# Performance work log

Measured on AMD Instinct MI355X. Metric: run time of the kernel, lower is better.

Reference implementation:

```python
import jax, jax.numpy as jnp
import numpy as np


def _quantize(mat):
    # per-row (last-dim) symmetric int8 quantization; scale stored in fp16 like torch
    max_val = (jnp.max(jnp.abs(mat), axis=-1) / 127.0).astype(jnp.float16)
    # torch's .to(int8) truncates toward zero; jnp astype does the same for in-range values
    q = (mat / max_val[..., None].astype(mat.dtype)).astype(jnp.int8)
    return q, max_val


def setup_inputs() -> dict:
    key = jax.random.key(0)
    k1, k2, k3, k4 = jax.random.split(key, 4)
    B, S, D_IN, D_OUT = 4, 2048, 4096, 4096
    x = jax.random.normal(k1, (B, S, D_IN), dtype=jnp.float32)
    origin_weight = jax.random.normal(k2, (D_OUT, D_IN), dtype=jnp.float32) * 0.02
    bias = jax.random.normal(k3, (D_OUT,), dtype=jnp.float32) * 0.01
    act_max = jax.random.normal(k4, (D_IN,), dtype=jnp.float32)
    return {"x": x, "origin_weight": origin_weight, "bias": bias,
            "act_max": act_max, "alpha": 32}


def reference(x, origin_weight, bias, act_max, alpha):
    d_in = act_max.shape[-1]
    # get_unq_idx_topk: top-alpha outlier channels by |act_max|
    _, idx = jax.lax.top_k(jnp.abs(act_max), alpha)          # [alpha]
    t = jnp.ones((d_in,), dtype=origin_weight.dtype).at[idx].set(0)

    # weight decomposition + quantization (done in __init__ in torch)
    weight_q, w_max = _quantize(origin_weight * t)           # [out,in] int8, [out] fp16
    weight_unq = origin_weight[:, idx].T                      # [alpha, out]

    # activation decomposition + per-token quantization
    x_unq = x[..., idx]                                       # [B,S,alpha]
    x_q, x_max = _quantize(x * t.astype(x.dtype))             # [B,S,in] int8, [B,S] fp16

    # simulated MatMulInteger: int8 values multiplied in fp32
    res_q = jnp.matmul(x_q.astype(jnp.float32), weight_q.T.astype(jnp.float32))  # [B,S,out]
    mx = (x_max[..., None] * w_max[None, :]).astype(jnp.float32)                  # [B,S,out]
    res_q = (res_q * mx).astype(x.dtype)

    # fp outlier path
    res_unq = jnp.matmul(x_unq, weight_unq) + bias
    return res_q + res_unq
```

## Files before the change

### kernel.cpp

```cpp
#include <hip/hip_runtime.h>
#include <hip/hip_fp16.h>

typedef __attribute__((ext_vector_type(4)))  int   i32x4;
typedef __attribute__((ext_vector_type(16))) int   i32x16;

#define ALPHA 32
#define BM 256
#define BN 128
#define BK 128


__global__ __launch_bounds__(256) void topk_kernel(const float* __restrict__ act_max,
                                                   int* __restrict__ idx_out,
                                                   unsigned* __restrict__ tbits,
                                                   int K) {
  __shared__ float v[4096];
  __shared__ float rv[4];
  __shared__ int   ri[4];
  __shared__ unsigned bits[128];
  const int t = threadIdx.x;
  for (int i = t; i < K; i += 256) v[i] = fabsf(act_max[i]);
  for (int i = t; i < K / 32; i += 256) bits[i] = 0xFFFFFFFFu;
  __syncthreads();
  for (int sel = 0; sel < ALPHA; ++sel) {
    float bv = -1.f; int bi = 0;
    for (int i = t; i < K; i += 256) {
      float x = v[i];
      if (x > bv) { bv = x; bi = i; }
    }
    for (int m = 1; m < 64; m <<= 1) {
      float ov = __shfl_xor(bv, m);
      int   oi = __shfl_xor(bi, m);
      if (ov > bv || (ov == bv && oi < bi)) { bv = ov; bi = oi; }
    }
    if ((t & 63) == 0) { rv[t >> 6] = bv; ri[t >> 6] = bi; }
    __syncthreads();
    if (t == 0) {
      for (int u = 1; u < 4; ++u)
        if (rv[u] > bv || (rv[u] == bv && ri[u] < bi)) { bv = rv[u]; bi = ri[u]; }
      idx_out[sel] = bi;
      v[bi] = -2.f;
      bits[bi >> 5] &= ~(1u << (bi & 31));
    }
    __syncthreads();
  }
  for (int i = t; i < K / 32; i += 256) tbits[i] = bits[i];
}

__global__ __launch_bounds__(256) void quant_rows_kernel(
    const float* __restrict__ src, const unsigned* __restrict__ tbits,
    const int* __restrict__ idx, signed char* __restrict__ q,
    _Float16* __restrict__ smax, float* __restrict__ unq, int K, int R) {
  __shared__ unsigned bits[128];
  __shared__ float red[4];
  const int t = threadIdx.x;
  const int r = blockIdx.x;
  for (int i = t; i < K / 32; i += 256) bits[i] = tbits[i];
  __syncthreads();
  const float4* srow = (const float4*)(src + (size_t)r * K);
  float4 vals[4];
  float am = 0.f;
#pragma unroll
  for (int j = 0; j < 4; ++j) {
    int p = 4 * t + j;
    float4 v = srow[p];
    int k0 = p << 2;
    unsigned b = bits[k0 >> 5] >> (k0 & 31);
    if (!(b & 1u)) v.x = 0.f;
    if (!(b & 2u)) v.y = 0.f;
    if (!(b & 4u)) v.z = 0.f;
    if (!(b & 8u)) v.w = 0.f;
    vals[j] = v;
    am = fmaxf(am, fmaxf(fmaxf(fabsf(v.x), fabsf(v.y)), fmaxf(fabsf(v.z), fabsf(v.w))));
  }
#pragma unroll
  for (int m = 1; m < 64; m <<= 1) am = fmaxf(am, __shfl_xor(am, m));
  if ((t & 63) == 0) red[t >> 6] = am;
  __syncthreads();
  am = fmaxf(fmaxf(red[0], red[1]), fmaxf(red[2], red[3]));
  const _Float16 sh = (_Float16)(am / 127.0f);
  const float s = (float)sh;
  if (t == 0) smax[r] = sh;
  union { signed char c[16]; int4 v; } o;
#pragma unroll
  for (int j = 0; j < 4; ++j) {
    float4 v = vals[j];
    o.c[4 * j + 0] = (signed char)(v.x / s);
    o.c[4 * j + 1] = (signed char)(v.y / s);
    o.c[4 * j + 2] = (signed char)(v.z / s);
    o.c[4 * j + 3] = (signed char)(v.w / s);
  }
  *(int4*)(q + (size_t)(r >> 5) * 32 * K + (size_t)t * 512 + (r & 31) * 16) = o.v;
  if (t < ALPHA) unq[(size_t)t * R + r] = src[(size_t)r * K + idx[t]];
}

__device__ __forceinline__ void gld_lds16(const signed char* g, signed char* l) {
  __builtin_amdgcn_global_load_lds(
      (const __attribute__((address_space(1))) void*)g,
      (__attribute__((address_space(3))) void*)l, 16, 0, 0);
}

__global__ __launch_bounds__(256, 2) void gemm_kernel(
    const signed char* __restrict__ xq, const signed char* __restrict__ wq,
    const _Float16* __restrict__ xmax, const _Float16* __restrict__ wmax,
    const float* __restrict__ xuf,
    const float* __restrict__ wuf,
    const float* __restrict__ bias,
    float* __restrict__ out, int M, int N, int K) {
  __shared__ union {
    struct { signed char A[BM * BK]; signed char B[BN * BK]; } g;
    struct { float xu[ALPHA * BM]; float wu[ALPHA * BN]; } e;
  } sm;
  __shared__ _Float16 xmh[BM];
  __shared__ _Float16 wmh[BN];
  __shared__ float    bl[BN];

  const int t = threadIdx.x;
  const int bid = blockIdx.y * gridDim.x + blockIdx.x;
  const int xcd = bid & 7, loc = bid >> 3;
  const int bxi = xcd * 4 + (loc & 3);
  const int byi = loc >> 2;
  const int bm0 = byi * BM;
  const int bn0 = bxi * BN;
  const int lane = t & 63, w = t >> 6;
  const int wm = w >> 1, wn = w & 1;
  const int hi = lane >> 5, l31 = lane & 31;

  i32x16 acc[4][2] = {};

  const signed char* aSrc = xq + (size_t)bm0 * K + 16 * t;
  const signed char* bSrc = wq + (size_t)bn0 * K + 16 * t;
  signed char* aDst = sm.g.A + t * 16;
  signed char* bDst = sm.g.B + t * 16;

  for (int k0 = 0; k0 < K; k0 += BK) {
    __syncthreads();
    const size_t koff = (size_t)k0 * 32;
#pragma unroll
    for (int i = 0; i < 8; ++i) gld_lds16(aSrc + (size_t)i * 32 * K + koff, aDst + i * 4096);
#pragma unroll
    for (int i = 0; i < 4; ++i) gld_lds16(bSrc + (size_t)i * 32 * K + koff, bDst + i * 4096);
    __syncthreads();
    const signed char* aRd = sm.g.A + 16 * lane + 4096 * (wm * 4);
    const signed char* bRd = sm.g.B + 16 * lane + 4096 * (wn * 2);
#pragma unroll
    for (int ks = 0; ks < 4; ++ks) {
      i32x4 af[4], bf[2];
#pragma unroll
      for (int mi = 0; mi < 4; ++mi)
        af[mi] = *(const i32x4*)(aRd + mi * 4096 + ks * 1024);
#pragma unroll
      for (int ni = 0; ni < 2; ++ni)
        bf[ni] = *(const i32x4*)(bRd + ni * 4096 + ks * 1024);
#pragma unroll
      for (int mi = 0; mi < 4; ++mi)
#pragma unroll
        for (int ni = 0; ni < 2; ++ni)
          acc[mi][ni] = __builtin_amdgcn_mfma_i32_32x32x32_i8(af[mi], bf[ni], acc[mi][ni], 0, 0, 0);
    }
  }

  __syncthreads();
  {
    const float4* xs = (const float4*)xuf;
    float4* xl = (float4*)sm.e.xu;
#pragma unroll
    for (int i = 0; i < 8; ++i) {
      int p = i * 256 + t;
      int j = p >> 6, r4 = p & 63;
      xl[p] = xs[(size_t)j * (M >> 2) + (bm0 >> 2) + r4];
    }
    const float4* wsrc = (const float4*)wuf;
    float4* wl = (float4*)sm.e.wu;
#pragma unroll
    for (int i = 0; i < 4; ++i) {
      int p = i * 256 + t;
      int j = p >> 5, r4 = p & 31;
      wl[p] = wsrc[(size_t)j * (N >> 2) + (bn0 >> 2) + r4];
    }
    if (t < BM / 2) ((unsigned*)xmh)[t] = ((const unsigned*)(xmax + bm0))[t];
    if (t < BN / 2) ((unsigned*)wmh)[t] = ((const unsigned*)(wmax + bn0))[t];
    if (t < BN / 4) ((float4*)bl)[t] = ((const float4*)(bias + bn0))[t];
  }
  __syncthreads();

  const int c0 = wn * 64 + l31;
  const _Float16 wh0 = wmh[c0], wh1 = wmh[c0 + 32];
  const float bv0 = bl[c0], bv1 = bl[c0 + 32];
  const float* xul = sm.e.xu;
  const float* wul = sm.e.wu;

#pragma unroll
  for (int mi = 0; mi < 4; ++mi) {
    const int rbase = wm * 128 + mi * 32 + 4 * hi;
    float f0[16], f1[16];
#pragma unroll
    for (int r = 0; r < 16; ++r) {
      int row = rbase + (r & 3) + 8 * (r >> 2);
      _Float16 xh = xmh[row];
      float mx0 = (float)(_Float16)(xh * wh0);
      float mx1 = (float)(_Float16)(xh * wh1);
      f0[r] = (float)acc[mi][0][r] * mx0 + bv0;
      f1[r] = (float)acc[mi][1][r] * mx1 + bv1;
    }
#pragma unroll 4
    for (int j = 0; j < ALPHA; ++j) {
      const float4* xrow4 = (const float4*)(xul + j * BM + rbase);
      float wv0 = wul[j * BN + c0];
      float wv1 = wul[j * BN + c0 + 32];
#pragma unroll
      for (int gq = 0; gq < 4; ++gq) {
        float4 xv = xrow4[gq * 2];
        f0[gq * 4 + 0] += xv.x * wv0;  f1[gq * 4 + 0] += xv.x * wv1;
        f0[gq * 4 + 1] += xv.y * wv0;  f1[gq * 4 + 1] += xv.y * wv1;
        f0[gq * 4 + 2] += xv.z * wv0;  f1[gq * 4 + 2] += xv.z * wv1;
        f0[gq * 4 + 3] += xv.w * wv0;  f1[gq * 4 + 3] += xv.w * wv1;
      }
    }
#pragma unroll
    for (int r = 0; r < 16; ++r) {
      int row = bm0 + rbase + (r & 3) + 8 * (r >> 2);
      size_t o = (size_t)row * N + bn0;
      out[o + c0] = f0[r];
      out[o + c0 + 32] = f1[r];
    }
  }
}

extern "C" void kernel_launch(void* const* d_in, const int* in_sizes, int n_in,
                              void* d_out, int out_size, void* d_ws, size_t ws_size,
                              hipStream_t stream) {
  const float* x       = (const float*)d_in[0];
  const float* W       = (const float*)d_in[1];
  const float* bias    = (const float*)d_in[2];
  const float* act_max = (const float*)d_in[3];
  const int K = in_sizes[3];
  const int N = in_sizes[1] / K;
  const int M = in_sizes[0] / K;
  float* out = (float*)d_out;

  char* ws = (char*)d_ws;
  size_t off = 0;
  auto take = [&](size_t b) { char* p = ws + off; off += (b + 255) & ~(size_t)255; return p; };
  signed char* wq  = (signed char*)take((size_t)N * K);
  signed char* xq  = (signed char*)take((size_t)M * K);
  _Float16* wmax   = (_Float16*)take((size_t)N * 2);
  _Float16* xmax   = (_Float16*)take((size_t)M * 2);
  float* wuf       = (float*)take((size_t)ALPHA * N * 4);
  float* xuf       = (float*)take((size_t)ALPHA * M * 4);
  int* idx         = (int*)take(ALPHA * 4);
  unsigned* tbits  = (unsigned*)take((size_t)(K / 32) * 4);

  topk_kernel<<<1, 256, 0, stream>>>(act_max, idx, tbits, K);
  quant_rows_kernel<<<N, 256, 0, stream>>>(W, tbits, idx, wq, wmax, wuf, K, N);
  quant_rows_kernel<<<M, 256, 0, stream>>>(x, tbits, idx, xq, xmax, xuf, K, M);
  dim3 grid(N / BN, M / BM);
  gemm_kernel<<<grid, 256, 0, stream>>>(xq, wq, xmax, wmax, xuf, wuf, bias, out, M, N, K);
}
```

Before: 311.9 us.

## Double-buffer GEMM K-loop and merge quantization into one panel kernel

The GEMM main loop now uses two LDS buffers with BK halved to 64, so the next tile's global-to-LDS loads are issued before the current tile's MFMAs. It also replaces the two per-row quantization launches with one kernel where each 1024-thread block handles a 32-row panel of W or x. That kernel writes the quantized bytes through an XOR-swizzled LDS staging buffer so global stores go out as full 16-byte lines. The aim is to hide memory latency in the GEMM and cut launch count and uncoalesced int8 stores, at the cost of more LDS per block and raw waitcnt/barrier asm that must stay correct.

```diff
diff --git a/kernel.cpp b/kernel.cpp
--- a/kernel.cpp
+++ b/kernel.cpp
@@ -7,7 +7,7 @@
 #define ALPHA 32
 #define BM 256
 #define BN 128
-#define BK 128
+#define BK 64
 
 
 __global__ __launch_bounds__(256) void topk_kernel(const float* __restrict__ act_max,
@@ -47,51 +47,76 @@
   for (int i = t; i < K / 32; i += 256) tbits[i] = bits[i];
 }
 
-__global__ __launch_bounds__(256) void quant_rows_kernel(
-    const float* __restrict__ src, const unsigned* __restrict__ tbits,
-    const int* __restrict__ idx, signed char* __restrict__ q,
-    _Float16* __restrict__ smax, float* __restrict__ unq, int K, int R) {
+__global__ __launch_bounds__(1024) void quant_panel_kernel(
+    const float* __restrict__ srcW, const float* __restrict__ srcX,
+    const unsigned* __restrict__ tbits, const int* __restrict__ idx,
+    signed char* __restrict__ wq, signed char* __restrict__ xq,
+    _Float16* __restrict__ wmax, _Float16* __restrict__ xmax,
+    float* __restrict__ wuf, float* __restrict__ xuf,
+    int npw, int K, int N, int M) {
+  const int t = threadIdx.x;
+  const int b = blockIdx.x;
+  const float* src; signed char* q; _Float16* smax; float* unq; int r0, R;
+  if (b < npw) { src = srcW; q = wq; smax = wmax; unq = wuf; r0 = b * 32; R = N; }
+  else         { src = srcX; q = xq; smax = xmax; unq = xuf; r0 = (b - npw) * 32; R = M; }
   __shared__ unsigned bits[128];
-  __shared__ float red[4];
-  const int t = threadIdx.x;
-  const int r = blockIdx.x;
-  for (int i = t; i < K / 32; i += 256) bits[i] = tbits[i];
+  __shared__ float wred[8][16];
+  __shared__ float scs[8];
+  __shared__ signed char qt[8 * 4096];
+  const int lane = t & 63, w = t >> 6;
+  for (int i = t; i < K / 32; i += 1024) bits[i] = tbits[i];
   __syncthreads();
-  const float4* srow = (const float4*)(src + (size_t)r * K);
-  float4 vals[4];
-  float am = 0.f;
-#pragma unroll
-  for (int j = 0; j < 4; ++j) {
-    int p = 4 * t + j;
-    float4 v = srow[p];
-    int k0 = p << 2;
-    unsigned b = bits[k0 >> 5] >> (k0 & 31);
-    if (!(b & 1u)) v.x = 0.f;
-    if (!(b & 2u)) v.y = 0.f;
-    if (!(b & 4u)) v.z = 0.f;
-    if (!(b & 8u)) v.w = 0.f;
-    vals[j] = v;
-    am = fmaxf(am, fmaxf(fmaxf(fabsf(v.x), fabsf(v.y)), fmaxf(fabsf(v.z), fabsf(v.w))));
-  }
-#pragma unroll
-  for (int m = 1; m < 64; m <<= 1) am = fmaxf(am, __shfl_xor(am, m));
-  if ((t & 63) == 0) red[t >> 6] = am;
-  __syncthreads();
-  am = fmaxf(fmaxf(red[0], red[1]), fmaxf(red[2], red[3]));
-  const _Float16 sh = (_Float16)(am / 127.0f);
-  const float s = (float)sh;
-  if (t == 0) smax[r] = sh;
-  union { signed char c[16]; int4 v; } o;
-#pragma unroll
-  for (int j = 0; j < 4; ++j) {
-    float4 v = vals[j];
-    o.c[4 * j + 0] = (signed char)(v.x / s);
-    o.c[4 * j + 1] = (signed char)(v.y / s);
-    o.c[4 * j + 2] = (signed char)(v.z / s);
-    o.c[4 * j + 3] = (signed char)(v.w / s);
-  }
-  *(int4*)(q + (size_t)(r >> 5) * 32 * K + (size_t)t * 512 + (r & 31) * 16) = o.v;
-  if (t < ALPHA) unq[(size_t)t * R + r] = src[(size_t)r * K + idx[t]];
+  const int k0 = t * 4;
+  const unsigned bw = bits[k0 >> 5] >> (k0 & 31);
+  const bool m0 = bw & 1u, m1 = bw & 2u, m2 = bw & 4u, m3 = bw & 8u;
+  const size_t pbase = (size_t)r0 * K;
+  for (int g = 0; g < 4; ++g) {
+    float4 v[8];
+#pragma unroll
+    for (int i = 0; i < 8; ++i) {
+      float4 x = ((const float4*)(src + (size_t)(r0 + g * 8 + i) * K))[t];
+      if (!m0) x.x = 0.f; if (!m1) x.y = 0.f; if (!m2) x.z = 0.f; if (!m3) x.w = 0.f;
+      v[i] = x;
+      float am = fmaxf(fmaxf(fabsf(x.x), fabsf(x.y)), fmaxf(fabsf(x.z), fabsf(x.w)));
+#pragma unroll
+      for (int m = 1; m < 64; m <<= 1) am = fmaxf(am, __shfl_xor(am, m));
+      if (lane == 0) wred[i][w] = am;
+    }
+    __syncthreads();
+    if (t < 8) {
+      float am = wred[t][0];
+#pragma unroll
+      for (int u = 1; u < 16; ++u) am = fmaxf(am, wred[t][u]);
+      _Float16 sh = (_Float16)(am / 127.0f);
+      scs[t] = (float)sh;
+      smax[r0 + g * 8 + t] = sh;
+    }
+    __syncthreads();
+    const int cc = t >> 2, sub = (t & 3) * 4;
+#pragma unroll
+    for (int i = 0; i < 8; ++i) {
+      const float s = scs[i];
+      char4 c;
+      c.x = (signed char)(v[i].x / s);
+      c.y = (signed char)(v[i].y / s);
+      c.z = (signed char)(v[i].z / s);
+      c.w = (signed char)(v[i].w / s);
+      *(char4*)(qt + cc * 128 + ((i ^ (cc & 7)) << 4) + sub) = c;
+    }
+    __syncthreads();
+#pragma unroll
+    for (int i = 0; i < 2; ++i) {
+      const int l = i * 1024 + t;
+      const int c2 = l >> 3, rl = l & 7;
+      int4 d = *(const int4*)(qt + c2 * 128 + ((rl ^ (c2 & 7)) << 4));
+      *(int4*)(q + pbase + (size_t)c2 * 512 + (size_t)((g * 8 + rl) << 4)) = d;
+    }
+    __syncthreads();
+  }
+  {
+    const int j = t >> 5, rl = t & 31;
+    unq[(size_t)j * R + r0 + rl] = src[(size_t)(r0 + rl) * K + idx[j]];
+  }
 }
 
 __device__ __forceinline__ void gld_lds16(const signed char* g, signed char* l) {
@@ -108,7 +133,7 @@
     const float* __restrict__ bias,
     float* __restrict__ out, int M, int N, int K) {
   __shared__ union {
-    struct { signed char A[BM * BK]; signed char B[BN * BK]; } g;
+    struct { signed char A[2][BM * BK]; signed char B[2][BN * BK]; } g;
     struct { float xu[ALPHA * BM]; float wu[ALPHA * BN]; } e;
   } sm;
   __shared__ _Float16 xmh[BM];
@@ -128,36 +153,53 @@
 
   i32x16 acc[4][2] = {};
 
-  const signed char* aSrc = xq + (size_t)bm0 * K + 16 * t;
-  const signed char* bSrc = wq + (size_t)bn0 * K + 16 * t;
-  signed char* aDst = sm.g.A + t * 16;
-  signed char* bDst = sm.g.B + t * 16;
-
-  for (int k0 = 0; k0 < K; k0 += BK) {
-    __syncthreads();
-    const size_t koff = (size_t)k0 * 32;
-#pragma unroll
-    for (int i = 0; i < 8; ++i) gld_lds16(aSrc + (size_t)i * 32 * K + koff, aDst + i * 4096);
-#pragma unroll
-    for (int i = 0; i < 4; ++i) gld_lds16(bSrc + (size_t)i * 32 * K + koff, bDst + i * 4096);
-    __syncthreads();
-    const signed char* aRd = sm.g.A + 16 * lane + 4096 * (wm * 4);
-    const signed char* bRd = sm.g.B + 16 * lane + 4096 * (wn * 2);
-#pragma unroll
-    for (int ks = 0; ks < 4; ++ks) {
-      i32x4 af[4], bf[2];
+  const int tp = t >> 7;
+  const int to = (t & 127) * 16;
+  const signed char* aS = xq + (size_t)bm0 * K + (size_t)tp * 32 * K + to;
+  const signed char* bS = wq + (size_t)bn0 * K + (size_t)tp * 32 * K + to;
+  signed char* const aD = &sm.g.A[0][0] + t * 16;
+  signed char* const bD = &sm.g.B[0][0] + t * 16;
+  const size_t PSTR = (size_t)64 * K;
+
+  auto STAGE = [&](int buf, int kt) {
+    const size_t ko = (size_t)kt * 2048;
+#pragma unroll
+    for (int i = 0; i < 4; ++i)
+      gld_lds16(aS + (size_t)i * PSTR + ko, aD + buf * (BM * BK) + i * 4096);
+#pragma unroll
+    for (int i = 0; i < 2; ++i)
+      gld_lds16(bS + (size_t)i * PSTR + ko, bD + buf * (BN * BK) + i * 4096);
+  };
+
+  STAGE(0, 0);
+  const int NT = K >> 6;
+  const signed char* const aR0 = &sm.g.A[0][0] + (wm * 4) * 2048 + 16 * lane;
+  const signed char* const bR0 = &sm.g.B[0][0] + (wn * 2) * 2048 + 16 * lane;
+
+  for (int kt = 0; kt < NT; ++kt) {
+    const int cur = kt & 1;
+    asm volatile("s_waitcnt vmcnt(0)" ::: "memory");
+    asm volatile("s_barrier" ::: "memory");
+    const signed char* aRd = aR0 + cur * (BM * BK);
+    const signed char* bRd = bR0 + cur * (BN * BK);
+    i32x4 af[2][4], bf[2][2];
+#pragma unroll
+    for (int ks = 0; ks < 2; ++ks) {
+#pragma unroll
+      for (int mi = 0; mi < 4; ++mi) af[ks][mi] = *(const i32x4*)(aRd + mi * 2048 + ks * 1024);
+#pragma unroll
+      for (int ni = 0; ni < 2; ++ni) bf[ks][ni] = *(const i32x4*)(bRd + ni * 2048 + ks * 1024);
+    }
+    if (kt + 1 < NT) STAGE(cur ^ 1, kt + 1);
+    __builtin_amdgcn_s_setprio(1);
+#pragma unroll
+    for (int ks = 0; ks < 2; ++ks)
 #pragma unroll
       for (int mi = 0; mi < 4; ++mi)
-        af[mi] = *(const i32x4*)(aRd + mi * 4096 + ks * 1024);
-#pragma unroll
-      for (int ni = 0; ni < 2; ++ni)
-        bf[ni] = *(const i32x4*)(bRd + ni * 4096 + ks * 1024);
-#pragma unroll
-      for (int mi = 0; mi < 4; ++mi)
 #pragma unroll
         for (int ni = 0; ni < 2; ++ni)
-          acc[mi][ni] = __builtin_amdgcn_mfma_i32_32x32x32_i8(af[mi], bf[ni], acc[mi][ni], 0, 0, 0);
-    }
+          acc[mi][ni] = __builtin_amdgcn_mfma_i32_32x32x32_i8(af[ks][mi], bf[ks][ni], acc[mi][ni], 0, 0, 0);
+    __builtin_amdgcn_s_setprio(0);
   }
 
   __syncthreads();
@@ -251,9 +293,10 @@
   int* idx         = (int*)take(ALPHA * 4);
   unsigned* tbits  = (unsigned*)take((size_t)(K / 32) * 4);
 
+  const int npw = N / 32, npx = M / 32;
   topk_kernel<<<1, 256, 0, stream>>>(act_max, idx, tbits, K);
-  quant_rows_kernel<<<N, 256, 0, stream>>>(W, tbits, idx, wq, wmax, wuf, K, N);
-  quant_rows_kernel<<<M, 256, 0, stream>>>(x, tbits, idx, xq, xmax, xuf, K, M);
+  quant_panel_kernel<<<npw + npx, 1024, 0, stream>>>(W, x, tbits, idx, wq, xq,
+                                                     wmax, xmax, wuf, xuf, npw, K, N, M);
   dim3 grid(N / BN, M / BM);
   gemm_kernel<<<grid, 256, 0, stream>>>(xq, wq, xmax, wmax, xuf, wuf, bias, out, M, N, K);
 }
```

Result: no change. 315.6 us (+1.2%).
